# Kernel optimization log

Measured on AMD Instinct MI355X. Metric: run time of the kernel, lower is better.

The kernel has to match this reference:

```python
import jax, jax.numpy as jnp
import numpy as np

EMB = 1024
HEADS = 16
HEAD_DIM = EMB // HEADS
EPS = 1e-5


def layer_norm(x, scale, shift):
    mean = jnp.mean(x, axis=-1, keepdims=True)
    var = jnp.mean(jnp.square(x - mean), axis=-1, keepdims=True)  # unbiased=False
    return scale * ((x - mean) / jnp.sqrt(var + EPS)) + shift


def gelu_tanh(x):
    c = jnp.sqrt(jnp.asarray(2.0 / jnp.pi, x.dtype))
    return 0.5 * x * (1.0 + jnp.tanh(c * (x + 0.044715 * x * x * x)))


def setup_inputs() -> dict:
    key = jax.random.key(0)
    ks = jax.random.split(key, 12)
    s = 0.02
    B, S, D = 2, 2048, EMB
    return {
        "x": jax.random.normal(ks[0], (B, S, D), jnp.float32),
        "wq": jax.random.normal(ks[1], (D, D), jnp.float32) * s,
        "wk": jax.random.normal(ks[2], (D, D), jnp.float32) * s,
        "wv": jax.random.normal(ks[3], (D, D), jnp.float32) * s,
        "wo": jax.random.normal(ks[4], (D, D), jnp.float32) * s,
        "bo": jnp.zeros((D,), jnp.float32),
        "w1": jax.random.normal(ks[5], (D, 4 * D), jnp.float32) * s,
        "b1": jnp.zeros((4 * D,), jnp.float32),
        "w2": jax.random.normal(ks[6], (4 * D, D), jnp.float32) * s,
        "b2": jnp.zeros((D,), jnp.float32),
        "g1": jnp.ones((D,), jnp.float32),
        "s1": jnp.zeros((D,), jnp.float32),
        "g2": jnp.ones((D,), jnp.float32),
        "s2": jnp.zeros((D,), jnp.float32),
    }


def reference(x, wq, wk, wv, wo, bo, w1, b1, w2, b2, g1, s1, g2, s2):
    B, S, D = x.shape
    # --- attention sub-block ---
    h = layer_norm(x, g1, s1)
    q = (h @ wq).reshape(B, S, HEADS, HEAD_DIM).transpose(0, 2, 1, 3)  # [B,H,S,d]
    k = (h @ wk).reshape(B, S, HEADS, HEAD_DIM).transpose(0, 2, 1, 3)
    v = (h @ wv).reshape(B, S, HEADS, HEAD_DIM).transpose(0, 2, 1, 3)
    scores = jnp.einsum("bhqd,bhkd->bhqk", q, k)
    causal = jnp.tril(jnp.ones((S, S), bool))  # True = keep
    scores = jnp.where(causal, scores, -jnp.inf)
    attn = jax.nn.softmax(scores / jnp.sqrt(jnp.asarray(HEAD_DIM, x.dtype)), axis=-1)
    ctx = jnp.einsum("bhqk,bhkd->bhqd", attn, v).transpose(0, 2, 1, 3).reshape(B, S, D)
    x = x + (ctx @ wo + bo)
    # --- FFN sub-block ---
    h = layer_norm(x, g2, s2)
    h = gelu_tanh(h @ w1 + b1) @ w2 + b2
    return x + h
```

## Files before the change

### kernel.cpp

```cpp
#include <hip/hip_runtime.h>


typedef __attribute__((ext_vector_type(8))) short s16x8;
typedef __attribute__((ext_vector_type(4))) float f32x4;
typedef __attribute__((ext_vector_type(16))) float f32x16;
typedef unsigned short u16;
typedef unsigned int u32;

#define DEV static __device__ __forceinline__
#define MFMA16 __builtin_amdgcn_mfma_f32_16x16x32_bf16
#define MFMA32 __builtin_amdgcn_mfma_f32_32x32x16_bf16
#define GLOAD_LDS16(gp, lp)                                         \
  __builtin_amdgcn_global_load_lds(                                 \
      (const __attribute__((address_space(1))) void*)(gp),          \
      (__attribute__((address_space(3))) void*)(lp), 16, 0, 0)
#define WAIT_VM(N) asm volatile("s_waitcnt vmcnt(" #N ")" ::: "memory")

DEV u16 f2bf(float f) {
  union { float f; unsigned u; } c; c.f = f;
  unsigned u = c.u;
  u += 0x7fff + ((u >> 16) & 1);
  return (u16)(u >> 16);
}

DEV u32 cvtpk(float lo, float hi) {
  u32 r;
  asm("v_cvt_pk_bf16_f32 %0, %1, %2" : "=v"(r) : "v"(lo), "v"(hi));
  return r;
}

DEV float gelu_tanh(float v) {
  const float c0 = 0.7978845608028654f;
  float u = c0 * (v + 0.044715f * v * v * v);
  return 0.5f * v * (1.0f + tanhf(u));
}

DEV s16x8 ld8(const u16* p) { return *(const s16x8*)p; }

DEV void tconv_tile(const float* __restrict__ W, u16* __restrict__ Wt, int K,
                    int N, int bx, int by, int t) {
  __shared__ u16 T[64][80];
  const int n0 = bx * 64, k0 = by * 64;
  const int kr = t >> 4, nc = (t & 15) * 4;
#pragma unroll
  for (int p = 0; p < 4; ++p) {
    const int k = p * 16 + kr;
    float4 v = *(const float4*)(W + (size_t)(k0 + k) * N + n0 + nc);
    T[nc + 0][k] = f2bf(v.x);
    T[nc + 1][k] = f2bf(v.y);
    T[nc + 2][k] = f2bf(v.z);
    T[nc + 3][k] = f2bf(v.w);
  }
  __syncthreads();
  const int nr = t >> 2, kc = (t & 3) * 16;
  *(s16x8*)(Wt + (size_t)(n0 + nr) * K + k0 + kc) = *(const s16x8*)&T[nr][kc];
  *(s16x8*)(Wt + (size_t)(n0 + nr) * K + k0 + kc + 8) =
      *(const s16x8*)&T[nr][kc + 8];
}

__global__ __launch_bounds__(256) void tconv_all(
    const float* __restrict__ wq, const float* __restrict__ wk,
    const float* __restrict__ wv, const float* __restrict__ wo,
    const float* __restrict__ w1, const float* __restrict__ w2,
    u16* __restrict__ qkvw, u16* __restrict__ wot, u16* __restrict__ w1t,
    u16* __restrict__ w2t) {
  const int idx = blockIdx.x, t = threadIdx.x;
  if (idx < 768) {
    const int which = idx >> 8, r = idx & 255;
    const float* W = which == 0 ? wq : (which == 1 ? wk : wv);
    tconv_tile(W, qkvw + which * 1048576, 1024, 1024, r & 15, r >> 4, t);
  } else if (idx < 1024) {
    const int r = idx - 768;
    tconv_tile(wo, wot, 1024, 1024, r & 15, r >> 4, t);
  } else if (idx < 2048) {
    const int r = idx - 1024;
    tconv_tile(w1, w1t, 1024, 4096, r & 63, r >> 6, t);
  } else {
    const int r = idx - 2048;
    tconv_tile(w2, w2t, 4096, 1024, r & 15, r >> 4, t);
  }
}

__global__ __launch_bounds__(256) void ln_kernel(
    const float* __restrict__ x, const float* __restrict__ g,
    const float* __restrict__ b, u16* __restrict__ out) {
  const int row = blockIdx.x;
  const int t = threadIdx.x;
  const float* xr = x + (size_t)row * 1024;
  float4 v = *(const float4*)(xr + t * 4);
  float s = v.x + v.y + v.z + v.w;
  float ss = v.x * v.x + v.y * v.y + v.z * v.z + v.w * v.w;
#pragma unroll
  for (int off = 1; off < 64; off <<= 1) {
    s += __shfl_xor(s, off);
    ss += __shfl_xor(ss, off);
  }
  __shared__ float sb[4], ssb[4];
  const int w = t >> 6;
  if ((t & 63) == 0) { sb[w] = s; ssb[w] = ss; }
  __syncthreads();
  s = sb[0] + sb[1] + sb[2] + sb[3];
  ss = ssb[0] + ssb[1] + ssb[2] + ssb[3];
  const float mean = s * (1.0f / 1024.0f);
  const float var = ss * (1.0f / 1024.0f) - mean * mean;
  const float rstd = rsqrtf(var + 1e-5f);
  const int c = t * 4;
  ushort4 o;
  o.x = f2bf(g[c + 0] * ((v.x - mean) * rstd) + b[c + 0]);
  o.y = f2bf(g[c + 1] * ((v.y - mean) * rstd) + b[c + 1]);
  o.z = f2bf(g[c + 2] * ((v.z - mean) * rstd) + b[c + 2]);
  o.w = f2bf(g[c + 3] * ((v.w - mean) * rstd) + b[c + 3]);
  *(ushort4*)(out + (size_t)row * 1024 + c) = o;
}

DEV void stage128(const u16* __restrict__ A, const u16* __restrict__ Bt,
                  int bm, int bn, int K, int kof, u16 (*Al)[32],
                  u16 (*Bl)[32], int w, int lane) {
  const int srow = lane >> 2;
  const int scol = ((lane & 3) ^ ((lane >> 3) & 3)) * 8;
#pragma unroll
  for (int p = 0; p < 2; ++p) {
    const int r0 = (w * 2 + p) * 16;
    GLOAD_LDS16(A + (size_t)(bm + r0 + srow) * K + kof + scol, &Al[r0][0]);
    GLOAD_LDS16(Bt + (size_t)(bn + r0 + srow) * K + kof + scol, &Bl[r0][0]);
  }
}

DEV void step128(const u16 (*Al)[32], const u16 (*Bl)[32],
                 f32x4 (&acc)[4][4], int wm, int wn, int lr, int lg) {
  const int cs = (lg ^ ((lr >> 1) & 3)) * 8;
  s16x8 af[4], bf[4];
#pragma unroll
  for (int i = 0; i < 4; ++i) {
    af[i] = *(const s16x8*)&Al[wm + i * 16 + lr][cs];
    bf[i] = *(const s16x8*)&Bl[wn + i * 16 + lr][cs];
  }
#pragma unroll
  for (int i = 0; i < 4; ++i)
#pragma unroll
    for (int j = 0; j < 4; ++j)
      acc[i][j] = MFMA16(af[i], bf[j], acc[i][j], 0, 0, 0);
}

template <int EPI>
__global__ __launch_bounds__(256) void pipe128_kernel(
    const u16* __restrict__ A, const u16* __restrict__ Bt,
    const float* __restrict__ bias, const float* __restrict__ res,
    void* __restrict__ Cv, int M, int N, int K) {
  __shared__ __align__(16) u16 Al[3][128][32];
  __shared__ __align__(16) u16 Bl[3][128][32];
  const int t = threadIdx.x;
  const int lane = t & 63, w = t >> 6;
  const int wm = (w >> 1) * 64, wn = (w & 1) * 64;
  int bid = blockIdx.y * gridDim.x + blockIdx.x;
  const int q8 = (gridDim.x * gridDim.y) >> 3;
  bid = (bid & 7) * q8 + (bid >> 3);
  const int bm = (bid / gridDim.x) * 128, bn = (bid % gridDim.x) * 128;
  const int lr = lane & 15, lg = lane >> 4;
  f32x4 acc[4][4] = {};
  const int nkt = K >> 5;

  stage128(A, Bt, bm, bn, K, 0, Al[0], Bl[0], w, lane);
  stage128(A, Bt, bm, bn, K, 32, Al[1], Bl[1], w, lane);
  for (int kt = 0; kt < nkt; ++kt) {
    if (kt == nkt - 1) WAIT_VM(0);
    else               WAIT_VM(4);
    __builtin_amdgcn_s_barrier();
    if (kt + 2 < nkt) {
      const int nb = (kt + 2) % 3;
      stage128(A, Bt, bm, bn, K, (kt + 2) << 5, Al[nb], Bl[nb], w, lane);
    }
    step128(Al[kt % 3], Bl[kt % 3], acc, wm, wn, lr, lg);
  }

#pragma unroll
  for (int i = 0; i < 4; ++i) {
    const int row = bm + wm + i * 16 + lg * 4;
#pragma unroll
    for (int j = 0; j < 4; ++j) {
      const int col = bn + wn + j * 16 + lr;
      if (EPI == 0) {
        const int bb = row >> 11, sloc = row & 2047;
        const int which = col >> 10, n = col & 1023;
        const int hh = n >> 6, dd = n & 63;
        u16* qbuf = (u16*)Cv;
        if (which == 2) {
          ushort4 o;
          o.x = f2bf(acc[i][j][0]); o.y = f2bf(acc[i][j][1]);
          o.z = f2bf(acc[i][j][2]); o.w = f2bf(acc[i][j][3]);
          *(ushort4*)(qbuf + 8388608 +
                      (size_t)((bb * 16 + hh) * 64 + dd) * 2048 + sloc) = o;
        } else {
          const float sc = (which == 0) ? 0.18033688011112042f : 1.0f;
          u16* dst = qbuf + (size_t)which * 4194304 +
                     ((size_t)(bb * 16 + hh) * 2048 + sloc) * 64 + dd;
#pragma unroll
          for (int e = 0; e < 4; ++e) dst[(size_t)e * 64] = f2bf(acc[i][j][e] * sc);
        }
      } else {
        u16* C = (u16*)Cv;
        const float bs = bias[col];
#pragma unroll
        for (int e = 0; e < 4; ++e)
          C[(size_t)(row + e) * N + col] = f2bf(gelu_tanh(acc[i][j][e] + bs));
      }
    }
  }
}

DEV void stage64(const u16* __restrict__ A, const u16* __restrict__ Bt,
                 int bm, int bn, int K, int kof, u16 (*Al)[32],
                 u16 (*Bl)[32], int w, int lane) {
  const int srow = lane >> 2;
  const int scol = ((lane & 3) ^ ((lane >> 3) & 3)) * 8;
  const int r0 = w << 4;
  GLOAD_LDS16(A + (size_t)(bm + r0 + srow) * K + kof + scol, &Al[r0][0]);
  GLOAD_LDS16(Bt + (size_t)(bn + r0 + srow) * K + kof + scol, &Bl[r0][0]);
}

DEV void step64(const u16 (*Al)[32], const u16 (*Bl)[32],
                f32x4 (&acc)[2][2], int wm, int wn, int lr, int lg) {
  const int cs = (lg ^ ((lr >> 1) & 3)) * 8;
  s16x8 af[2], bf[2];
#pragma unroll
  for (int i = 0; i < 2; ++i) {
    af[i] = *(const s16x8*)&Al[wm + i * 16 + lr][cs];
    bf[i] = *(const s16x8*)&Bl[wn + i * 16 + lr][cs];
  }
#pragma unroll
  for (int i = 0; i < 2; ++i)
#pragma unroll
    for (int j = 0; j < 2; ++j)
      acc[i][j] = MFMA16(af[i], bf[j], acc[i][j], 0, 0, 0);
}

__global__ __launch_bounds__(256) void pipe64_kernel(
    const u16* __restrict__ A, const u16* __restrict__ Bt,
    const float* __restrict__ bias, const float* __restrict__ res,
    float* __restrict__ C, int M, int N, int K) {
  __shared__ __align__(16) u16 Al[3][64][32];
  __shared__ __align__(16) u16 Bl[3][64][32];
  const int t = threadIdx.x;
  const int lane = t & 63, w = t >> 6;
  const int wm = (w >> 1) * 32, wn = (w & 1) * 32;
  int bid = blockIdx.y * gridDim.x + blockIdx.x;
  const int q8 = (gridDim.x * gridDim.y) >> 3;
  bid = (bid & 7) * q8 + (bid >> 3);
  const int bm = (bid / gridDim.x) * 64, bn = (bid % gridDim.x) * 64;
  const int lr = lane & 15, lg = lane >> 4;
  f32x4 acc[2][2] = {};
  const int nkt = K >> 5;

  stage64(A, Bt, bm, bn, K, 0, Al[0], Bl[0], w, lane);
  stage64(A, Bt, bm, bn, K, 32, Al[1], Bl[1], w, lane);
  for (int kt = 0; kt < nkt; ++kt) {
    if (kt == nkt - 1) WAIT_VM(0);
    else               WAIT_VM(2);
    __builtin_amdgcn_s_barrier();
    if (kt + 2 < nkt) {
      const int nb = (kt + 2) % 3;
      stage64(A, Bt, bm, bn, K, (kt + 2) << 5, Al[nb], Bl[nb], w, lane);
    }
    step64(Al[kt % 3], Bl[kt % 3], acc, wm, wn, lr, lg);
  }

#pragma unroll
  for (int i = 0; i < 2; ++i) {
    const int row = bm + wm + i * 16 + lg * 4;
#pragma unroll
    for (int j = 0; j < 2; ++j) {
      const int col = bn + wn + j * 16 + lr;
      const float bs = bias[col];
#pragma unroll
      for (int e = 0; e < 4; ++e)
        C[(size_t)(row + e) * N + col] =
            acc[i][j][e] + bs + res[(size_t)(row + e) * N + col];
    }
  }
}

DEV float vmax16(const f32x16& v) {
  float a = fmaxf(v[0], v[1]), b = fmaxf(v[2], v[3]);
  float c = fmaxf(v[4], v[5]), d = fmaxf(v[6], v[7]);
  float e = fmaxf(v[8], v[9]), f = fmaxf(v[10], v[11]);
  float g = fmaxf(v[12], v[13]), h = fmaxf(v[14], v[15]);
  a = fmaxf(a, b); c = fmaxf(c, d); e = fmaxf(e, f); g = fmaxf(g, h);
  return fmaxf(fmaxf(a, c), fmaxf(e, g));
}
DEV float vsum16(const f32x16& v) {
  float a = v[0] + v[1], b = v[2] + v[3];
  float c = v[4] + v[5], d = v[6] + v[7];
  float e = v[8] + v[9], f = v[10] + v[11];
  float g = v[12] + v[13], h = v[14] + v[15];
  a += b; c += d; e += f; g += h;
  return (a + c) + (e + g);
}

struct A32 {
  s16x8 q[4];
  f32x16 o0, o1;
  float m, l;
};

template <int MODE>
DEV void body32(A32& st, int k0, const u16* Kb, const u16* Vb, int la,
                int hi) {
  s16x8 ka0[4], ka1[4];
#pragma unroll
  for (int c = 0; c < 4; ++c)
    ka0[c] = ld8(Kb + (size_t)(k0 + la) * 64 + c * 16 + hi * 8);
  if (MODE != 2)
#pragma unroll
    for (int c = 0; c < 4; ++c)
      ka1[c] = ld8(Kb + (size_t)(k0 + 32 + la) * 64 + c * 16 + hi * 8);
  f32x16 s0, s1;
#pragma unroll
  for (int r = 0; r < 16; ++r) { s0[r] = 0.f; s1[r] = 0.f; }
#pragma unroll
  for (int c = 0; c < 4; ++c) s0 = MFMA32(ka0[c], st.q[c], s0, 0, 0, 0);
  if (MODE != 2)
#pragma unroll
    for (int c = 0; c < 4; ++c) s1 = MFMA32(ka1[c], st.q[c], s1, 0, 0, 0);
  const int nkc = (MODE == 2) ? 2 : 4;
  s16x8 va0[4], va1[4];
#pragma unroll
  for (int kc = 0; kc < 4; ++kc)
    if (kc < nkc) {
      va0[kc] = ld8(Vb + (size_t)la * 2048 + k0 + kc * 16 + hi * 8);
      va1[kc] = ld8(Vb + (size_t)(32 + la) * 2048 + k0 + kc * 16 + hi * 8);
    }
  if (MODE == 1) {
#pragma unroll
    for (int r = 0; r < 16; ++r) {
      const int kl = (r & 3) + 8 * (r >> 2) + 4 * hi;
      if (kl > la) s1[r] = -INFINITY;
    }
  }
  if (MODE == 2) {
#pragma unroll
    for (int r = 0; r < 16; ++r) {
      const int kl = (r & 3) + 8 * (r >> 2) + 4 * hi;
      if (kl > la) s0[r] = -INFINITY;
    }
  }
  float mt = vmax16(s0);
  if (MODE != 2) mt = fmaxf(mt, vmax16(s1));
  mt = fmaxf(mt, __shfl_xor(mt, 32));
  const bool skip = __all(mt <= st.m + 8.0f) != 0;
  const float mn = skip ? st.m : fmaxf(st.m, mt);
  const float sf = skip ? 1.0f : exp2f(st.m - mn);
#pragma unroll
  for (int r = 0; r < 16; ++r) s0[r] = exp2f(s0[r] - mn);
  if (MODE != 2)
#pragma unroll
    for (int r = 0; r < 16; ++r) s1[r] = exp2f(s1[r] - mn);
  float rs = vsum16(s0);
  if (MODE != 2) rs += vsum16(s1);
  rs += __shfl_xor(rs, 32);
  st.l = skip ? (st.l + rs) : (st.l * sf + rs);
  st.m = mn;
  if (!skip) {
#pragma unroll
    for (int r = 0; r < 16; ++r) { st.o0[r] *= sf; st.o1[r] *= sf; }
  }
  const int nh = (MODE == 2) ? 1 : 2;
#pragma unroll
  for (int half = 0; half < nh; ++half) {
    u32 w[8];
#pragma unroll
    for (int i = 0; i < 8; ++i)
      w[i] = half ? cvtpk(s1[2 * i], s1[2 * i + 1])
                  : cvtpk(s0[2 * i], s0[2 * i + 1]);
#pragma unroll
    for (int kp = 0; kp < 2; ++kp) {
      const u32 w0 = w[4 * kp + 0], w1 = w[4 * kp + 1];
      const u32 w2 = w[4 * kp + 2], w3 = w[4 * kp + 3];
      const u32 t0 = hi ? w0 : w2, t1 = hi ? w1 : w3;
      const u32 x0 = (u32)__shfl_xor((int)t0, 32);
      const u32 x1 = (u32)__shfl_xor((int)t1, 32);
      union { u32 u[4]; s16x8 v; } bb;
      bb.u[0] = hi ? x0 : w0;
      bb.u[1] = hi ? x1 : w1;
      bb.u[2] = hi ? w2 : x0;
      bb.u[3] = hi ? w3 : x1;
      const int kc = half * 2 + kp;
      st.o0 = MFMA32(va0[kc], bb.v, st.o0, 0, 0, 0);
      st.o1 = MFMA32(va1[kc], bb.v, st.o1, 0, 0, 0);
    }
  }
}

DEV void a32_init(A32& st, const u16* Qbase, int qs, int la, int hi) {
#pragma unroll
  for (int c = 0; c < 4; ++c)
    st.q[c] = ld8(Qbase + (size_t)(qs + la) * 64 + c * 16 + hi * 8);
#pragma unroll
  for (int r = 0; r < 16; ++r) { st.o0[r] = 0.f; st.o1[r] = 0.f; }
  st.m = -INFINITY;
  st.l = 0.f;
}

DEV void a32_fin(const A32& st, u16* __restrict__ ctx, int bh, int qs, int la,
                 int hi) {
  const int bb = bh >> 4, hh = bh & 15;
  const float inv = 1.0f / st.l;
  u16* crow = ctx + (size_t)(bb * 2048 + qs + la) * 1024 + hh * 64;
#pragma unroll
  for (int r = 0; r < 16; r += 2) {
    const int d = (r & 3) + 8 * (r >> 2) + 4 * hi;
    *(u32*)(crow + d) = cvtpk(st.o0[r] * inv, st.o0[r + 1] * inv);
    *(u32*)(crow + 32 + d) = cvtpk(st.o1[r] * inv, st.o1[r + 1] * inv);
  }
}

template <bool ODD>
DEV void chain_tail(A32& st, int nfull, int qs, const u16* Kb, const u16* Vb,
                    int la, int hi) {
  if (ODD) body32<1>(st, nfull * 64, Kb, Vb, la, hi);
  else     body32<2>(st, qs, Kb, Vb, la, hi);
}

__global__ __launch_bounds__(64) void attn_kernel(
    const u16* __restrict__ Qg, const u16* __restrict__ Kg,
    const u16* __restrict__ Vt, u16* __restrict__ ctx) {
  const int lane = threadIdx.x & 63;
  const int la = lane & 31, hi = lane >> 5;
  const int tA = blockIdx.x;
  const int bh = blockIdx.y;
  const int tB = 63 - tA;
  const int qsA = tA * 32, qsB = tB * 32;
  const int nfA = tA >> 1, nfB = tB >> 1;
  const size_t baseK = (size_t)bh * 2048 * 64;
  const size_t baseV = (size_t)bh * 64 * 2048;
  const u16* Kb = Kg + baseK;
  const u16* Vb = Vt + baseV;

  A32 A, B;
  a32_init(A, Qg + baseK, qsA, la, hi);
  a32_init(B, Qg + baseK, qsB, la, hi);

  for (int kt = 0; kt < nfA; ++kt) {
    body32<0>(B, kt * 64, Kb, Vb, la, hi);
    body32<0>(A, kt * 64, Kb, Vb, la, hi);
  }
  body32<0>(B, nfA * 64, Kb, Vb, la, hi);
  if (tA & 1) chain_tail<true>(A, nfA, qsA, Kb, Vb, la, hi);
  else        chain_tail<false>(A, nfA, qsA, Kb, Vb, la, hi);
  a32_fin(A, ctx, bh, qsA, la, hi);

  for (int kt = nfA + 1; kt < nfB; ++kt)
    body32<0>(B, kt * 64, Kb, Vb, la, hi);
  if (tB & 1) chain_tail<true>(B, nfB, qsB, Kb, Vb, la, hi);
  else        chain_tail<false>(B, nfB, qsB, Kb, Vb, la, hi);
  a32_fin(B, ctx, bh, qsB, la, hi);
}

extern "C" void kernel_launch(void* const* d_in, const int* in_sizes, int n_in,
                              void* d_out, int out_size, void* d_ws,
                              size_t ws_size, hipStream_t stream) {
  const float* x  = (const float*)d_in[0];
  const float* wq = (const float*)d_in[1];
  const float* wk = (const float*)d_in[2];
  const float* wv = (const float*)d_in[3];
  const float* wo = (const float*)d_in[4];
  const float* bo = (const float*)d_in[5];
  const float* w1 = (const float*)d_in[6];
  const float* b1 = (const float*)d_in[7];
  const float* w2 = (const float*)d_in[8];
  const float* b2 = (const float*)d_in[9];
  const float* g1 = (const float*)d_in[10];
  const float* s1 = (const float*)d_in[11];
  const float* g2 = (const float*)d_in[12];
  const float* s2 = (const float*)d_in[13];
  float* out = (float*)d_out;

  const size_t MB = (size_t)1 << 20;
  char* p = (char*)d_ws;
  u16* hb    = (u16*)(p + 0 * MB);
  u16* qbuf  = (u16*)(p + 8 * MB);
  u16* ctxb  = (u16*)(p + 32 * MB);
  float* x2  = (float*)(p + 40 * MB);
  u16* h2b   = (u16*)(p + 56 * MB);
  u16* qkvw  = (u16*)(p + 64 * MB);
  u16* wot   = (u16*)(p + 70 * MB);
  u16* w1t   = (u16*)(p + 72 * MB);
  u16* w2t   = (u16*)(p + 80 * MB);
  u16* gb    = (u16*)(p + 0 * MB);

  const dim3 blk(256);
  tconv_all<<<dim3(3072), blk, 0, stream>>>(wq, wk, wv, wo, w1, w2, qkvw, wot,
                                            w1t, w2t);
  ln_kernel<<<4096, blk, 0, stream>>>(x, g1, s1, hb);
  pipe128_kernel<0><<<dim3(24, 32), blk, 0, stream>>>(
      hb, qkvw, nullptr, nullptr, qbuf, 4096, 3072, 1024);
  attn_kernel<<<dim3(32, 32), dim3(64), 0, stream>>>(
      qbuf, qbuf + 4194304, qbuf + 8388608, ctxb);
  pipe64_kernel<<<dim3(16, 64), blk, 0, stream>>>(ctxb, wot, bo, x, x2, 4096,
                                                  1024, 1024);
  ln_kernel<<<4096, blk, 0, stream>>>(x2, g2, s2, h2b);
  pipe128_kernel<2><<<dim3(32, 32), blk, 0, stream>>>(
      h2b, w1t, b1, nullptr, gb, 4096, 4096, 1024);
  pipe64_kernel<<<dim3(16, 64), blk, 0, stream>>>(gb, w2t, b2, x2, out, 4096,
                                                  1024, 4096);
}
```

Before: 302.8 us.

## Software-pipeline K/V tile loads in registers and share tiles across paired query blocks

Adds a double-buffered register prefetch of the next 64-key K and V tile while the current tile is computed, and shares each loaded tile between the two paired query blocks instead of reloading it per block. It also drops the lazy-rescale skip in the online softmax, so the accumulator is always rescaled. The aim is to hide global-load latency and halve redundant K/V loads, at the cost of much higher register pressure from the two tile buffers plus two accumulator states, which could spill or lower occupancy.

```diff
diff --git a/kernel.cpp b/kernel.cpp
--- a/kernel.cpp
+++ b/kernel.cpp
@@ -302,6 +302,67 @@
   float m, l;
 };
 
+struct TileRegs { s16x8 k0[4], k1[4], v0[4], v1[4]; };
+
+DEV void tld(TileRegs& r, int k0, const u16* Kb, const u16* Vb, int la,
+             int hi) {
+#pragma unroll
+  for (int c = 0; c < 4; ++c) {
+    r.k0[c] = ld8(Kb + (size_t)(k0 + la) * 64 + c * 16 + hi * 8);
+    r.k1[c] = ld8(Kb + (size_t)(k0 + 32 + la) * 64 + c * 16 + hi * 8);
+    r.v0[c] = ld8(Vb + (size_t)la * 2048 + k0 + c * 16 + hi * 8);
+    r.v1[c] = ld8(Vb + (size_t)(32 + la) * 2048 + k0 + c * 16 + hi * 8);
+  }
+}
+
+DEV void bcomp0(A32& st, const TileRegs& tr, int la, int hi) {
+  f32x16 s0, s1;
+#pragma unroll
+  for (int r = 0; r < 16; ++r) { s0[r] = 0.f; s1[r] = 0.f; }
+#pragma unroll
+  for (int c = 0; c < 4; ++c) s0 = MFMA32(tr.k0[c], st.q[c], s0, 0, 0, 0);
+#pragma unroll
+  for (int c = 0; c < 4; ++c) s1 = MFMA32(tr.k1[c], st.q[c], s1, 0, 0, 0);
+  float mt = fmaxf(vmax16(s0), vmax16(s1));
+  mt = fmaxf(mt, __shfl_xor(mt, 32));
+  const float mn = fmaxf(st.m, mt);
+  const float sf = exp2f(st.m - mn);
+#pragma unroll
+  for (int r = 0; r < 16; ++r) s0[r] = exp2f(s0[r] - mn);
+#pragma unroll
+  for (int r = 0; r < 16; ++r) s1[r] = exp2f(s1[r] - mn);
+  float rs = vsum16(s0) + vsum16(s1);
+  rs += __shfl_xor(rs, 32);
+  st.l = st.l * sf + rs;
+  st.m = mn;
+#pragma unroll
+  for (int r = 0; r < 16; ++r) { st.o0[r] *= sf; st.o1[r] *= sf; }
+#pragma unroll
+  for (int half = 0; half < 2; ++half) {
+    u32 w[8];
+#pragma unroll
+    for (int i = 0; i < 8; ++i)
+      w[i] = half ? cvtpk(s1[2 * i], s1[2 * i + 1])
+                  : cvtpk(s0[2 * i], s0[2 * i + 1]);
+#pragma unroll
+    for (int kp = 0; kp < 2; ++kp) {
+      const u32 w0 = w[4 * kp + 0], w1 = w[4 * kp + 1];
+      const u32 w2 = w[4 * kp + 2], w3 = w[4 * kp + 3];
+      const u32 t0 = hi ? w0 : w2, t1 = hi ? w1 : w3;
+      const u32 x0 = (u32)__shfl_xor((int)t0, 32);
+      const u32 x1 = (u32)__shfl_xor((int)t1, 32);
+      union { u32 u[4]; s16x8 v; } bb;
+      bb.u[0] = hi ? x0 : w0;
+      bb.u[1] = hi ? x1 : w1;
+      bb.u[2] = hi ? w2 : x0;
+      bb.u[3] = hi ? w3 : x1;
+      const int kc = half * 2 + kp;
+      st.o0 = MFMA32(tr.v0[kc], bb.v, st.o0, 0, 0, 0);
+      st.o1 = MFMA32(tr.v1[kc], bb.v, st.o1, 0, 0, 0);
+    }
+  }
+}
+
 template <int MODE>
 DEV void body32(A32& st, int k0, const u16* Kb, const u16* Vb, int la,
                 int hi) {
@@ -346,9 +407,8 @@
   float mt = vmax16(s0);
   if (MODE != 2) mt = fmaxf(mt, vmax16(s1));
   mt = fmaxf(mt, __shfl_xor(mt, 32));
-  const bool skip = __all(mt <= st.m + 8.0f) != 0;
-  const float mn = skip ? st.m : fmaxf(st.m, mt);
-  const float sf = skip ? 1.0f : exp2f(st.m - mn);
+  const float mn = fmaxf(st.m, mt);
+  const float sf = exp2f(st.m - mn);
 #pragma unroll
   for (int r = 0; r < 16; ++r) s0[r] = exp2f(s0[r] - mn);
   if (MODE != 2)
@@ -357,12 +417,10 @@
   float rs = vsum16(s0);
   if (MODE != 2) rs += vsum16(s1);
   rs += __shfl_xor(rs, 32);
-  st.l = skip ? (st.l + rs) : (st.l * sf + rs);
+  st.l = st.l * sf + rs;
   st.m = mn;
-  if (!skip) {
-#pragma unroll
-    for (int r = 0; r < 16; ++r) { st.o0[r] *= sf; st.o1[r] *= sf; }
-  }
+#pragma unroll
+  for (int r = 0; r < 16; ++r) { st.o0[r] *= sf; st.o1[r] *= sf; }
   const int nh = (MODE == 2) ? 1 : 2;
 #pragma unroll
   for (int half = 0; half < nh; ++half) {
@@ -413,13 +471,6 @@
   }
 }
 
-template <bool ODD>
-DEV void chain_tail(A32& st, int nfull, int qs, const u16* Kb, const u16* Vb,
-                    int la, int hi) {
-  if (ODD) body32<1>(st, nfull * 64, Kb, Vb, la, hi);
-  else     body32<2>(st, qs, Kb, Vb, la, hi);
-}
-
 __global__ __launch_bounds__(64) void attn_kernel(
     const u16* __restrict__ Qg, const u16* __restrict__ Kg,
     const u16* __restrict__ Vt, u16* __restrict__ ctx) {
@@ -439,19 +490,26 @@
   a32_init(A, Qg + baseK, qsA, la, hi);
   a32_init(B, Qg + baseK, qsB, la, hi);
 
-  for (int kt = 0; kt < nfA; ++kt) {
-    body32<0>(B, kt * 64, Kb, Vb, la, hi);
-    body32<0>(A, kt * 64, Kb, Vb, la, hi);
-  }
-  body32<0>(B, nfA * 64, Kb, Vb, la, hi);
-  if (tA & 1) chain_tail<true>(A, nfA, qsA, Kb, Vb, la, hi);
-  else        chain_tail<false>(A, nfA, qsA, Kb, Vb, la, hi);
+  TileRegs r0, r1;
+  tld(r0, 0, Kb, Vb, la, hi);
+  int kt = 0;
+  while (kt < nfB) {
+    if (kt + 1 < nfB) tld(r1, (kt + 1) * 64, Kb, Vb, la, hi);
+    bcomp0(B, r0, la, hi);
+    if (kt < nfA) bcomp0(A, r0, la, hi);
+    ++kt;
+    if (kt >= nfB) break;
+    if (kt + 1 < nfB) tld(r0, (kt + 1) * 64, Kb, Vb, la, hi);
+    bcomp0(B, r1, la, hi);
+    if (kt < nfA) bcomp0(A, r1, la, hi);
+    ++kt;
+  }
+
+  if (tA & 1) body32<1>(A, nfA * 64, Kb, Vb, la, hi);
+  else        body32<2>(A, nfA * 64, Kb, Vb, la, hi);
+  if (tB & 1) body32<1>(B, nfB * 64, Kb, Vb, la, hi);
+  else        body32<2>(B, nfB * 64, Kb, Vb, la, hi);
   a32_fin(A, ctx, bh, qsA, la, hi);
-
-  for (int kt = nfA + 1; kt < nfB; ++kt)
-    body32<0>(B, kt * 64, Kb, Vb, la, hi);
-  if (tB & 1) chain_tail<true>(B, nfB, qsB, Kb, Vb, la, hi);
-  else        chain_tail<false>(B, nfB, qsB, Kb, Vb, la, hi);
   a32_fin(B, ctx, bh, qsB, la, hi);
 }
 
```

New measurement: 281.7 us. 1.07x faster.
